# Kernel tuning notes

Measured on AMD Instinct MI355X. Metric: run time of the kernel, lower is better.

Reference implementation:

```python
import jax, jax.numpy as jnp
import numpy as np

NUM_HEADS = 16
THRESHOLD = 0.1  # default forward arg; with seq_len > 2**max_qubits the Grover path degenerates to probs > threshold


def setup_inputs() -> dict:
    key = jax.random.key(0)
    ks = jax.random.split(key, 5)
    B, S, E = 4, 1024, 1024
    return {
        "x": jax.random.normal(ks[0], (B, S, E), dtype=jnp.float32),
        "w_qkv": jax.random.normal(ks[1], (E, 3 * E), dtype=jnp.float32) * (E ** -0.5),
        "b_qkv": jax.random.normal(ks[2], (3 * E,), dtype=jnp.float32) * 0.02,
        "w_proj": jax.random.normal(ks[3], (E, E), dtype=jnp.float32) * (E ** -0.5),
        "b_proj": jax.random.normal(ks[4], (E,), dtype=jnp.float32) * 0.02,
    }


def reference(x, w_qkv, b_qkv, w_proj, b_proj):
    B, S, E = x.shape
    H = NUM_HEADS
    Dh = E // H
    scale = Dh ** -0.5
    # qkv projection -> [3, B, H, S, Dh]
    qkv = (x @ w_qkv + b_qkv).reshape(B, S, 3, H, Dh).transpose(2, 0, 3, 1, 4)
    q, k, v = qkv[0], qkv[1], qkv[2]
    attn_logits = jnp.einsum("bhqd,bhkd->bhqk", q, k) * scale  # [B,H,S,S]
    attn_probs = jax.nn.softmax(attn_logits, axis=-1)
    # Grover filter degenerates to threshold mask for S > 2**max_qubits
    mask = attn_probs > THRESHOLD
    any_selected = jnp.any(mask, axis=-1, keepdims=True)
    # fallback: keep only the argmax column in rows where nothing passed threshold
    fallback = jax.nn.one_hot(jnp.argmax(attn_probs, axis=-1), S, dtype=jnp.bool_)
    mask = jnp.where(any_selected, mask, fallback)
    filtered_logits = jnp.where(mask, attn_logits, -jnp.inf)
    filtered_attn = jax.nn.softmax(filtered_logits, axis=-1)
    # dropout is identity in eval / p=0
    out = jnp.einsum("bhqk,bhkd->bhqd", filtered_attn, v)  # [B,H,S,Dh]
    out = out.transpose(0, 2, 1, 3).reshape(B, S, E)
    out = out @ w_proj + b_proj
    return out, filtered_attn
```

## Files before the change

kernel.cpp:

```cpp
#include <hip/hip_runtime.h>
#include <math.h>

#define SS 1024
#define OUT0_SZ (4*1024*1024)

typedef _Float16 f16;
typedef _Float16 h8 __attribute__((ext_vector_type(8)));
typedef _Float16 h4 __attribute__((ext_vector_type(4)));
typedef float f32x4 __attribute__((ext_vector_type(4)));

#define MFMA(a,b,c) __builtin_amdgcn_mfma_f32_16x16x32_f16(a, b, c, 0, 0, 0)

__device__ __forceinline__ void gload_lds16(const void* g, void* l) {
  __builtin_amdgcn_global_load_lds((const __attribute__((address_space(1))) void*)g,
                                   (__attribute__((address_space(3))) void*)l, 16, 0, 0);
}

template<int SPLIT>
__global__ __launch_bounds__(256)
void transpose_split(const float* __restrict__ in, f16* __restrict__ outHi,
                     f16* __restrict__ outLo, int K, int N, float scale) {
  __shared__ float t[32][33];
  const int n0 = blockIdx.x * 32, k0 = blockIdx.y * 32;
  const int tx = threadIdx.x & 31, ty = threadIdx.x >> 5;
#pragma unroll
  for (int j = 0; j < 4; j++)
    t[ty + j * 8][tx] = in[(size_t)(k0 + ty + j * 8) * N + n0 + tx] * scale;
  __syncthreads();
#pragma unroll
  for (int j = 0; j < 4; j++) {
    float v = t[tx][ty + j * 8];
    f16 h = (f16)v;
    size_t idx = (size_t)(n0 + ty + j * 8) * K + k0 + tx;
    outHi[idx] = h;
    if (SPLIT) outLo[idx] = (f16)(v - (float)h);
  }
}

__global__ __launch_bounds__(256)
void transpose_v(const f16* __restrict__ in, f16* __restrict__ out) {
  __shared__ f16 t[32][33];
  const int bh = blockIdx.z, s0 = blockIdx.x * 32, d0 = blockIdx.y * 32;
  in  += (size_t)bh * 65536;
  out += (size_t)bh * 65536;
  const int tx = threadIdx.x & 31, ty = threadIdx.x >> 5;
#pragma unroll
  for (int j = 0; j < 4; j++)
    t[ty + j * 8][tx] = in[(size_t)(s0 + ty + j * 8) * 64 + d0 + tx];
  __syncthreads();
#pragma unroll
  for (int j = 0; j < 4; j++)
    out[(size_t)(d0 + ty + j * 8) * 1024 + s0 + tx] = t[tx][ty + j * 8];
}

__global__ __launch_bounds__(256)
void qkv_gemm(const float* __restrict__ x, const f16* __restrict__ WhiT,
              const f16* __restrict__ WloT, const float* __restrict__ bias,
              f16* __restrict__ Qhi, f16* __restrict__ Qlo,
              f16* __restrict__ Khi, f16* __restrict__ Klo, f16* __restrict__ Vf) {
  __shared__ __align__(16) f16 Ah[128 * 32], Al[128 * 32], Bh[128 * 32], Bl[128 * 32];
  const int tid = threadIdx.x, w = tid >> 6, l = tid & 63;
  const int n0 = blockIdx.x * 128, m0 = blockIdx.y * 128;
  const int wr = (w & 1) * 64, wc = (w >> 1) * 64;
  const int fr = l & 15, fq = l >> 4;
  f32x4 acc[4][4] = {};

  for (int kt = 0; kt < 1024; kt += 32) {
    __syncthreads();
#pragma unroll
    for (int i = 0; i < 2; i++) {
      int row = w * 32 + i * 16 + (l >> 2);
      size_t srcoff = (size_t)(n0 + row) * 1024 + kt + (l & 3) * 8;
      gload_lds16(WhiT + srcoff, Bh + w * 1024 + i * 512);
      gload_lds16(WloT + srcoff, Bl + w * 1024 + i * 512);
    }
#pragma unroll
    for (int r4 = 0; r4 < 4; r4++) {
      int f = r4 * 256 + tid;
      int row = f >> 3, c4 = (f & 7) * 4;
      float4 xv = *(const float4*)&x[(size_t)(m0 + row) * 1024 + kt + c4];
      float vv[4] = {xv.x, xv.y, xv.z, xv.w};
      h4 hh, ll;
#pragma unroll
      for (int j = 0; j < 4; j++) {
        float sv = vv[j] * 64.f;
        f16 h = (f16)sv;
        hh[j] = h; ll[j] = (f16)(sv - (float)h);
      }
      *(h4*)&Ah[row * 32 + c4] = hh;
      *(h4*)&Al[row * 32 + c4] = ll;
    }
    __syncthreads();
    h8 ah[4], al[4], bh[4], bl[4];
#pragma unroll
    for (int m = 0; m < 4; m++) {
      ah[m] = *(h8*)&Ah[(wr + m * 16 + fr) * 32 + fq * 8];
      al[m] = *(h8*)&Al[(wr + m * 16 + fr) * 32 + fq * 8];
    }
#pragma unroll
    for (int n = 0; n < 4; n++) {
      bh[n] = *(h8*)&Bh[(wc + n * 16 + fr) * 32 + fq * 8];
      bl[n] = *(h8*)&Bl[(wc + n * 16 + fr) * 32 + fq * 8];
    }
#pragma unroll
    for (int m = 0; m < 4; m++)
#pragma unroll
      for (int n = 0; n < 4; n++) {
        acc[m][n] = MFMA(ah[m], bh[n], acc[m][n]);
        acc[m][n] = MFMA(al[m], bh[n], acc[m][n]);
        acc[m][n] = MFMA(ah[m], bl[n], acc[m][n]);
      }
  }

#pragma unroll
  for (int m = 0; m < 4; m++)
#pragma unroll
    for (int n = 0; n < 4; n++)
#pragma unroll
      for (int j = 0; j < 4; j++) {
        int row = m0 + wr + m * 16 + fq * 4 + j;
        int col = n0 + wc + n * 16 + fr;
        float val = acc[m][n][j] * (1.f / 262144.f) + bias[col];
        int t = col >> 10, h = (col >> 6) & 15, d = col & 63;
        int b = row >> 10, s = row & 1023;
        size_t idx = ((size_t)(b * 16 + h) * 1024 + s) * 64 + d;
        if (t == 0) { f16 hh = (f16)(val * 64.f); Qhi[idx] = hh; Qlo[idx] = (f16)(val * 64.f - (float)hh); }
        else if (t == 1) { f16 hh = (f16)(val * 64.f); Khi[idx] = hh; Klo[idx] = (f16)(val * 64.f - (float)hh); }
        else Vf[idx] = (f16)val;
      }
}

__global__ __launch_bounds__(256)
void qk_gemm(const f16* __restrict__ Qhi, const f16* __restrict__ Qlo,
             const f16* __restrict__ Khi, const f16* __restrict__ Klo,
             float* __restrict__ att) {
  __shared__ __align__(16) f16 Ah[128 * 32], Al[128 * 32], Bh[128 * 32], Bl[128 * 32];
  const int bh = blockIdx.z;
  const size_t off = (size_t)bh * 65536;
  const int tid = threadIdx.x, w = tid >> 6, l = tid & 63;
  const int n0 = blockIdx.x * 128, m0 = blockIdx.y * 128;
  const int wr = (w & 1) * 64, wc = (w >> 1) * 64;
  const int fr = l & 15, fq = l >> 4;
  f32x4 acc[4][4] = {};

  for (int kt = 0; kt < 64; kt += 32) {
    __syncthreads();
#pragma unroll
    for (int i = 0; i < 2; i++) {
      int row = w * 32 + i * 16 + (l >> 2);
      int co = kt + (l & 3) * 8;
      gload_lds16(Qhi + off + (size_t)(m0 + row) * 64 + co, Ah + w * 1024 + i * 512);
      gload_lds16(Qlo + off + (size_t)(m0 + row) * 64 + co, Al + w * 1024 + i * 512);
      gload_lds16(Khi + off + (size_t)(n0 + row) * 64 + co, Bh + w * 1024 + i * 512);
      gload_lds16(Klo + off + (size_t)(n0 + row) * 64 + co, Bl + w * 1024 + i * 512);
    }
    __syncthreads();
    h8 ah[4], al[4], bh[4], bl[4];
#pragma unroll
    for (int m = 0; m < 4; m++) {
      ah[m] = *(h8*)&Ah[(wr + m * 16 + fr) * 32 + fq * 8];
      al[m] = *(h8*)&Al[(wr + m * 16 + fr) * 32 + fq * 8];
    }
#pragma unroll
    for (int n = 0; n < 4; n++) {
      bh[n] = *(h8*)&Bh[(wc + n * 16 + fr) * 32 + fq * 8];
      bl[n] = *(h8*)&Bl[(wc + n * 16 + fr) * 32 + fq * 8];
    }
#pragma unroll
    for (int m = 0; m < 4; m++)
#pragma unroll
      for (int n = 0; n < 4; n++) {
        acc[m][n] = MFMA(ah[m], bh[n], acc[m][n]);
        acc[m][n] = MFMA(al[m], bh[n], acc[m][n]);
        acc[m][n] = MFMA(ah[m], bl[n], acc[m][n]);
      }
  }

  float* L = att + (size_t)bh * 1048576;
#pragma unroll
  for (int m = 0; m < 4; m++)
#pragma unroll
    for (int n = 0; n < 4; n++)
#pragma unroll
      for (int j = 0; j < 4; j++) {
        int row = m0 + wr + m * 16 + fq * 4 + j;
        int col = n0 + wc + n * 16 + fr;
        L[(size_t)row * 1024 + col] = acc[m][n][j] * (1.f / 32768.f);
      }
}

__global__ __launch_bounds__(256)
void softmax_filter(float* __restrict__ att) {
  float* p = att + (size_t)blockIdx.x * SS;
  const int tid = threadIdx.x;
  const int lane = tid & 63, wv = tid >> 6;

  float4 z4 = *(const float4*)&p[tid * 4];
  float z[4] = {z4.x, z4.y, z4.z, z4.w};

  float m = z[0]; int am = tid * 4;
#pragma unroll
  for (int j = 1; j < 4; j++) if (z[j] > m) { m = z[j]; am = tid * 4 + j; }
#pragma unroll
  for (int off = 32; off >= 1; off >>= 1) {
    float om = __shfl_xor(m, off, 64);
    int oa = __shfl_xor(am, off, 64);
    if (om > m || (om == m && oa < am)) { m = om; am = oa; }
  }
  __shared__ float wm[4]; __shared__ int wa[4];
  __shared__ float wsum[4]; __shared__ float wf[4]; __shared__ int wany[4];
  if (lane == 0) { wm[wv] = m; wa[wv] = am; }
  __syncthreads();
  m = wm[0]; am = wa[0];
#pragma unroll
  for (int w = 1; w < 4; w++) {
    float om = wm[w]; int oa = wa[w];
    if (om > m || (om == m && oa < am)) { m = om; am = oa; }
  }

  float e[4]; float s = 0.f;
#pragma unroll
  for (int j = 0; j < 4; j++) { e[j] = expf(z[j] - m); s += e[j]; }
#pragma unroll
  for (int off = 32; off >= 1; off >>= 1) s += __shfl_xor(s, off, 64);
  if (lane == 0) wsum[wv] = s;
  __syncthreads();
  s = wsum[0] + wsum[1] + wsum[2] + wsum[3];

  bool sel[4]; float fl = 0.f; int anyl = 0;
#pragma unroll
  for (int j = 0; j < 4; j++) {
    sel[j] = (e[j] / s > 0.1f);
    if (sel[j]) { fl += e[j]; anyl = 1; }
  }
#pragma unroll
  for (int off = 32; off >= 1; off >>= 1) fl += __shfl_xor(fl, off, 64);
  int wany_l = __any(anyl);
  if (lane == 0) { wf[wv] = fl; wany[wv] = wany_l; }
  __syncthreads();
  float fs = wf[0] + wf[1] + wf[2] + wf[3];
  int any = wany[0] | wany[1] | wany[2] | wany[3];

  float4 fa;
  float* faf = (float*)&fa;
#pragma unroll
  for (int j = 0; j < 4; j++) {
    if (any) faf[j] = sel[j] ? e[j] / fs : 0.f;
    else     faf[j] = (tid * 4 + j == am) ? 1.f : 0.f;
  }
  *(float4*)&p[tid * 4] = fa;
}

__global__ __launch_bounds__(256)
void pv_gemm(const float* __restrict__ att, const f16* __restrict__ Vt,
             f16* __restrict__ ao) {
  __shared__ __align__(16) f16 A[128 * 32], B[64 * 32];
  const int bh = blockIdx.y, m0 = blockIdx.x * 128;
  const float* fa = att + (size_t)bh * 1048576;
  const f16* Vb = Vt + (size_t)bh * 65536;
  const int tid = threadIdx.x, w = tid >> 6, l = tid & 63;
  const int wr = (w & 1) * 64, wc = (w >> 1) * 32;
  const int fr = l & 15, fq = l >> 4;
  f32x4 acc[4][2] = {};

  for (int kt = 0; kt < 1024; kt += 32) {
    __syncthreads();
    {
      int row = w * 16 + (l >> 2);
      gload_lds16(Vb + (size_t)row * 1024 + kt + (l & 3) * 8, B + w * 512);
    }
#pragma unroll
    for (int r4 = 0; r4 < 4; r4++) {
      int f = r4 * 256 + tid;
      int row = f >> 3, c4 = (f & 7) * 4;
      float4 pv4 = *(const float4*)&fa[(size_t)(m0 + row) * 1024 + kt + c4];
      h4 hh;
      hh[0] = (f16)pv4.x; hh[1] = (f16)pv4.y; hh[2] = (f16)pv4.z; hh[3] = (f16)pv4.w;
      *(h4*)&A[row * 32 + c4] = hh;
    }
    __syncthreads();
    h8 a[4], b[2];
#pragma unroll
    for (int m = 0; m < 4; m++) a[m] = *(h8*)&A[(wr + m * 16 + fr) * 32 + fq * 8];
#pragma unroll
    for (int n = 0; n < 2; n++) b[n] = *(h8*)&B[(wc + n * 16 + fr) * 32 + fq * 8];
#pragma unroll
    for (int m = 0; m < 4; m++)
#pragma unroll
      for (int n = 0; n < 2; n++) acc[m][n] = MFMA(a[m], b[n], acc[m][n]);
  }

  const int b = bh >> 4, h = bh & 15;
#pragma unroll
  for (int m = 0; m < 4; m++)
#pragma unroll
    for (int n = 0; n < 2; n++)
#pragma unroll
      for (int j = 0; j < 4; j++) {
        int s = m0 + wr + m * 16 + fq * 4 + j;
        int d = wc + n * 16 + fr;
        ao[((size_t)(b * 1024 + s)) * 1024 + h * 64 + d] = (f16)acc[m][n][j];
      }
}

__global__ __launch_bounds__(256)
void proj_gemm(const f16* __restrict__ ao, const f16* __restrict__ WpT,
               const float* __restrict__ bias, float* __restrict__ out) {
  __shared__ __align__(16) f16 A[128 * 32], B[128 * 32];
  const int tid = threadIdx.x, w = tid >> 6, l = tid & 63;
  const int n0 = blockIdx.x * 128, m0 = blockIdx.y * 128;
  const int wr = (w & 1) * 64, wc = (w >> 1) * 64;
  const int fr = l & 15, fq = l >> 4;
  f32x4 acc[4][4] = {};

  for (int kt = 0; kt < 1024; kt += 32) {
    __syncthreads();
#pragma unroll
    for (int i = 0; i < 2; i++) {
      int row = w * 32 + i * 16 + (l >> 2);
      gload_lds16(ao  + (size_t)(m0 + row) * 1024 + kt + (l & 3) * 8, A + w * 1024 + i * 512);
      gload_lds16(WpT + (size_t)(n0 + row) * 1024 + kt + (l & 3) * 8, B + w * 1024 + i * 512);
    }
    __syncthreads();
    h8 a[4], b[4];
#pragma unroll
    for (int m = 0; m < 4; m++) a[m] = *(h8*)&A[(wr + m * 16 + fr) * 32 + fq * 8];
#pragma unroll
    for (int n = 0; n < 4; n++) b[n] = *(h8*)&B[(wc + n * 16 + fr) * 32 + fq * 8];
#pragma unroll
    for (int m = 0; m < 4; m++)
#pragma unroll
      for (int n = 0; n < 4; n++) acc[m][n] = MFMA(a[m], b[n], acc[m][n]);
  }

#pragma unroll
  for (int m = 0; m < 4; m++)
#pragma unroll
    for (int n = 0; n < 4; n++)
#pragma unroll
      for (int j = 0; j < 4; j++) {
        int row = m0 + wr + m * 16 + fq * 4 + j;
        int col = n0 + wc + n * 16 + fr;
        out[(size_t)row * 1024 + col] = acc[m][n][j] + bias[col];
      }
}

extern "C" void kernel_launch(void* const* d_in, const int* in_sizes, int n_in,
                              void* d_out, int out_size, void* d_ws, size_t ws_size,
                              hipStream_t stream) {
  const float* x      = (const float*)d_in[0];
  const float* w_qkv  = (const float*)d_in[1];
  const float* b_qkv  = (const float*)d_in[2];
  const float* w_proj = (const float*)d_in[3];
  const float* b_proj = (const float*)d_in[4];

  float* out0 = (float*)d_out;
  float* att  = out0 + OUT0_SZ;

  f16* ws16 = (f16*)d_ws;
  f16* WhiT = ws16;
  f16* WloT = ws16 +  3145728;
  f16* WpT  = ws16 +  6291456;
  f16* Qhi  = ws16 +  7340032;
  f16* Qlo  = ws16 + 11534336;
  f16* Khi  = ws16 + 15728640;
  f16* Klo  = ws16 + 19922944;
  f16* Vf   = ws16 + 24117248;
  f16* Vt   = ws16 + 28311552;
  f16* ao16 = ws16;

  transpose_split<1><<<dim3(96, 32), 256, 0, stream>>>(w_qkv, WhiT, WloT, 1024, 3072, 4096.f);
  transpose_split<0><<<dim3(32, 32), 256, 0, stream>>>(w_proj, WpT, nullptr, 1024, 1024, 1.f);
  qkv_gemm<<<dim3(24, 32), 256, 0, stream>>>(x, WhiT, WloT, b_qkv, Qhi, Qlo, Khi, Klo, Vf);
  transpose_v<<<dim3(32, 2, 64), 256, 0, stream>>>(Vf, Vt);
  qk_gemm<<<dim3(8, 8, 64), 256, 0, stream>>>(Qhi, Qlo, Khi, Klo, att);
  softmax_filter<<<64 * SS, 256, 0, stream>>>(att);
  pv_gemm<<<dim3(8, 64), 256, 0, stream>>>(att, Vt, ao16);
  proj_gemm<<<dim3(8, 32), 256, 0, stream>>>(ao16, WpT, b_proj, out0);
}
```

Before: 661.4 us.

## Fuse QK^T with softmax filter in LDS and pre-split x to fp16

Replaces the separate QK^T GEMM and row softmax/threshold kernels with one kernel. It computes a 32-row stripe of logits into LDS, using swizzled K tiles, and then does the softmax, threshold and argmax fallback in place before writing the attention matrix once. This removes a full fp32 write and re-read of the 256 MB logits tensor. Separately, x is split into hi/lo fp16 buffers by a new pre-kernel, staged in the attention output region, so qkv_gemm can use direct global-to-LDS loads instead of converting inside the loop. The fused kernel uses a large LDS footprint (about 148 KB), which limits occupancy.

```diff
diff --git a/kernel.cpp b/kernel.cpp
--- a/kernel.cpp
+++ b/kernel.cpp
@@ -38,6 +38,22 @@
 }
 
 __global__ __launch_bounds__(256)
+void splitx(const float* __restrict__ x, f16* __restrict__ hi, f16* __restrict__ lo) {
+  const size_t i4 = (size_t)blockIdx.x * 256 + threadIdx.x;
+  float4 v = ((const float4*)x)[i4];
+  float vv[4] = {v.x, v.y, v.z, v.w};
+  h4 hh, ll;
+#pragma unroll
+  for (int j = 0; j < 4; j++) {
+    float sv = vv[j] * 64.f;
+    f16 h = (f16)sv;
+    hh[j] = h; ll[j] = (f16)(sv - (float)h);
+  }
+  ((h4*)hi)[i4] = hh;
+  ((h4*)lo)[i4] = ll;
+}
+
+__global__ __launch_bounds__(256)
 void transpose_v(const f16* __restrict__ in, f16* __restrict__ out) {
   __shared__ f16 t[32][33];
   const int bh = blockIdx.z, s0 = blockIdx.x * 32, d0 = blockIdx.y * 32;
@@ -54,8 +70,9 @@
 }
 
 __global__ __launch_bounds__(256)
-void qkv_gemm(const float* __restrict__ x, const f16* __restrict__ WhiT,
-              const f16* __restrict__ WloT, const float* __restrict__ bias,
+void qkv_gemm(const f16* __restrict__ Xhi, const f16* __restrict__ Xlo,
+              const f16* __restrict__ WhiT, const f16* __restrict__ WloT,
+              const float* __restrict__ bias,
               f16* __restrict__ Qhi, f16* __restrict__ Qlo,
               f16* __restrict__ Khi, f16* __restrict__ Klo, f16* __restrict__ Vf) {
   __shared__ __align__(16) f16 Ah[128 * 32], Al[128 * 32], Bh[128 * 32], Bl[128 * 32];
@@ -70,25 +87,13 @@
 #pragma unroll
     for (int i = 0; i < 2; i++) {
       int row = w * 32 + i * 16 + (l >> 2);
-      size_t srcoff = (size_t)(n0 + row) * 1024 + kt + (l & 3) * 8;
-      gload_lds16(WhiT + srcoff, Bh + w * 1024 + i * 512);
-      gload_lds16(WloT + srcoff, Bl + w * 1024 + i * 512);
-    }
-#pragma unroll
-    for (int r4 = 0; r4 < 4; r4++) {
-      int f = r4 * 256 + tid;
-      int row = f >> 3, c4 = (f & 7) * 4;
-      float4 xv = *(const float4*)&x[(size_t)(m0 + row) * 1024 + kt + c4];
-      float vv[4] = {xv.x, xv.y, xv.z, xv.w};
-      h4 hh, ll;
-#pragma unroll
-      for (int j = 0; j < 4; j++) {
-        float sv = vv[j] * 64.f;
-        f16 h = (f16)sv;
-        hh[j] = h; ll[j] = (f16)(sv - (float)h);
-      }
-      *(h4*)&Ah[row * 32 + c4] = hh;
-      *(h4*)&Al[row * 32 + c4] = ll;
+      int co = kt + (l & 3) * 8;
+      size_t aoff = (size_t)(m0 + row) * 1024 + co;
+      size_t boff = (size_t)(n0 + row) * 1024 + co;
+      gload_lds16(Xhi  + aoff, Ah + w * 1024 + i * 512);
+      gload_lds16(Xlo  + aoff, Al + w * 1024 + i * 512);
+      gload_lds16(WhiT + boff, Bh + w * 1024 + i * 512);
+      gload_lds16(WloT + boff, Bl + w * 1024 + i * 512);
     }
     __syncthreads();
     h8 ah[4], al[4], bh[4], bl[4];
@@ -131,124 +136,102 @@
 }
 
 __global__ __launch_bounds__(256)
-void qk_gemm(const f16* __restrict__ Qhi, const f16* __restrict__ Qlo,
-             const f16* __restrict__ Khi, const f16* __restrict__ Klo,
-             float* __restrict__ att) {
-  __shared__ __align__(16) f16 Ah[128 * 32], Al[128 * 32], Bh[128 * 32], Bl[128 * 32];
-  const int bh = blockIdx.z;
+void qksm(const f16* __restrict__ Qhi, const f16* __restrict__ Qlo,
+          const f16* __restrict__ Khi, const f16* __restrict__ Klo,
+          float* __restrict__ att) {
+  __shared__ float P[32][1028];
+  __shared__ __align__(16) f16 KH[4096], KL[4096];
+  const int bh = blockIdx.y, m0 = blockIdx.x * 32;
   const size_t off = (size_t)bh * 65536;
   const int tid = threadIdx.x, w = tid >> 6, l = tid & 63;
-  const int n0 = blockIdx.x * 128, m0 = blockIdx.y * 128;
-  const int wr = (w & 1) * 64, wc = (w >> 1) * 64;
   const int fr = l & 15, fq = l >> 4;
-  f32x4 acc[4][4] = {};
-
-  for (int kt = 0; kt < 64; kt += 32) {
-    __syncthreads();
-#pragma unroll
-    for (int i = 0; i < 2; i++) {
-      int row = w * 32 + i * 16 + (l >> 2);
-      int co = kt + (l & 3) * 8;
-      gload_lds16(Qhi + off + (size_t)(m0 + row) * 64 + co, Ah + w * 1024 + i * 512);
-      gload_lds16(Qlo + off + (size_t)(m0 + row) * 64 + co, Al + w * 1024 + i * 512);
-      gload_lds16(Khi + off + (size_t)(n0 + row) * 64 + co, Bh + w * 1024 + i * 512);
-      gload_lds16(Klo + off + (size_t)(n0 + row) * 64 + co, Bl + w * 1024 + i * 512);
-    }
-    __syncthreads();
-    h8 ah[4], al[4], bh[4], bl[4];
-#pragma unroll
-    for (int m = 0; m < 4; m++) {
-      ah[m] = *(h8*)&Ah[(wr + m * 16 + fr) * 32 + fq * 8];
-      al[m] = *(h8*)&Al[(wr + m * 16 + fr) * 32 + fq * 8];
-    }
-#pragma unroll
-    for (int n = 0; n < 4; n++) {
-      bh[n] = *(h8*)&Bh[(wc + n * 16 + fr) * 32 + fq * 8];
-      bl[n] = *(h8*)&Bl[(wc + n * 16 + fr) * 32 + fq * 8];
-    }
-#pragma unroll
-    for (int m = 0; m < 4; m++)
-#pragma unroll
-      for (int n = 0; n < 4; n++) {
-        acc[m][n] = MFMA(ah[m], bh[n], acc[m][n]);
-        acc[m][n] = MFMA(al[m], bh[n], acc[m][n]);
-        acc[m][n] = MFMA(ah[m], bl[n], acc[m][n]);
-      }
-  }
-
-  float* L = att + (size_t)bh * 1048576;
-#pragma unroll
-  for (int m = 0; m < 4; m++)
-#pragma unroll
-    for (int n = 0; n < 4; n++)
-#pragma unroll
-      for (int j = 0; j < 4; j++) {
-        int row = m0 + wr + m * 16 + fq * 4 + j;
-        int col = n0 + wc + n * 16 + fr;
-        L[(size_t)row * 1024 + col] = acc[m][n][j] * (1.f / 32768.f);
-      }
-}
-
-__global__ __launch_bounds__(256)
-void softmax_filter(float* __restrict__ att) {
-  float* p = att + (size_t)blockIdx.x * SS;
-  const int tid = threadIdx.x;
-  const int lane = tid & 63, wv = tid >> 6;
-
-  float4 z4 = *(const float4*)&p[tid * 4];
-  float z[4] = {z4.x, z4.y, z4.z, z4.w};
-
-  float m = z[0]; int am = tid * 4;
-#pragma unroll
-  for (int j = 1; j < 4; j++) if (z[j] > m) { m = z[j]; am = tid * 4 + j; }
-#pragma unroll
-  for (int off = 32; off >= 1; off >>= 1) {
-    float om = __shfl_xor(m, off, 64);
-    int oa = __shfl_xor(am, off, 64);
-    if (om > m || (om == m && oa < am)) { m = om; am = oa; }
-  }
-  __shared__ float wm[4]; __shared__ int wa[4];
-  __shared__ float wsum[4]; __shared__ float wf[4]; __shared__ int wany[4];
-  if (lane == 0) { wm[wv] = m; wa[wv] = am; }
-  __syncthreads();
-  m = wm[0]; am = wa[0];
-#pragma unroll
-  for (int w = 1; w < 4; w++) {
-    float om = wm[w]; int oa = wa[w];
-    if (om > m || (om == m && oa < am)) { m = om; am = oa; }
-  }
-
-  float e[4]; float s = 0.f;
-#pragma unroll
-  for (int j = 0; j < 4; j++) { e[j] = expf(z[j] - m); s += e[j]; }
-#pragma unroll
-  for (int off = 32; off >= 1; off >>= 1) s += __shfl_xor(s, off, 64);
-  if (lane == 0) wsum[wv] = s;
-  __syncthreads();
-  s = wsum[0] + wsum[1] + wsum[2] + wsum[3];
-
-  bool sel[4]; float fl = 0.f; int anyl = 0;
-#pragma unroll
-  for (int j = 0; j < 4; j++) {
-    sel[j] = (e[j] / s > 0.1f);
-    if (sel[j]) { fl += e[j]; anyl = 1; }
-  }
-#pragma unroll
-  for (int off = 32; off >= 1; off >>= 1) fl += __shfl_xor(fl, off, 64);
-  int wany_l = __any(anyl);
-  if (lane == 0) { wf[wv] = fl; wany[wv] = wany_l; }
-  __syncthreads();
-  float fs = wf[0] + wf[1] + wf[2] + wf[3];
-  int any = wany[0] | wany[1] | wany[2] | wany[3];
-
-  float4 fa;
-  float* faf = (float*)&fa;
-#pragma unroll
-  for (int j = 0; j < 4; j++) {
-    if (any) faf[j] = sel[j] ? e[j] / fs : 0.f;
-    else     faf[j] = (tid * 4 + j == am) ? 1.f : 0.f;
-  }
-  *(float4*)&p[tid * 4] = fa;
+  const int nw = w * 16;
+
+  h8 qh[2][2], ql[2][2];
+#pragma unroll
+  for (int m = 0; m < 2; m++)
+#pragma unroll
+    for (int kk = 0; kk < 2; kk++) {
+      size_t o = off + (size_t)(m0 + 16 * m + fr) * 64 + kk * 32 + fq * 8;
+      qh[m][kk] = *(const h8*)(Qhi + o);
+      ql[m][kk] = *(const h8*)(Qlo + o);
+    }
+
+  const char* KhiB = (const char*)(Khi + off);
+  const char* KloB = (const char*)(Klo + off);
+
+  for (int c = 0; c < 16; c++) {
+    {
+      int i0 = w * 2;
+#pragma unroll
+      for (int i = i0; i < i0 + 2; i++) {
+        int r = i * 8 + (l >> 3);
+        size_t gb = (size_t)(c * 64 + r) * 128 + (size_t)(((l & 7) * 16) ^ ((r & 7) << 4));
+        gload_lds16(KhiB + gb, (char*)KH + i * 1024);
+        gload_lds16(KloB + gb, (char*)KL + i * 1024);
+      }
+    }
+    __syncthreads();
+    f32x4 acc[2] = {};
+    const int R = nw + fr;
+    const int rs = (R & 7) << 4;
+#pragma unroll
+    for (int kk = 0; kk < 2; kk++) {
+      h8 b_h = *(const h8*)((const char*)KH + R * 128 + ((kk * 64 + fq * 16) ^ rs));
+      h8 b_l = *(const h8*)((const char*)KL + R * 128 + ((kk * 64 + fq * 16) ^ rs));
+#pragma unroll
+      for (int m = 0; m < 2; m++) {
+        acc[m] = MFMA(qh[m][kk], b_h, acc[m]);
+        acc[m] = MFMA(ql[m][kk], b_h, acc[m]);
+        acc[m] = MFMA(qh[m][kk], b_l, acc[m]);
+      }
+    }
+#pragma unroll
+    for (int m = 0; m < 2; m++)
+#pragma unroll
+      for (int j = 0; j < 4; j++)
+        P[16 * m + fq * 4 + j][c * 64 + nw + fr] = acc[m][j] * (1.f / 32768.f);
+    __syncthreads();
+  }
+
+  const int r0 = w * 8;
+  for (int rr = 0; rr < 8; rr++) {
+    const int r = r0 + rr;
+    float z[16];
+#pragma unroll
+    for (int i = 0; i < 16; i++) z[i] = P[r][l + 64 * i];
+    float m = z[0]; int am = l;
+#pragma unroll
+    for (int i = 1; i < 16; i++) { int idx = l + 64 * i; if (z[i] > m) { m = z[i]; am = idx; } }
+#pragma unroll
+    for (int o = 32; o >= 1; o >>= 1) {
+      float om = __shfl_xor(m, o, 64);
+      int oa = __shfl_xor(am, o, 64);
+      if (om > m || (om == m && oa < am)) { m = om; am = oa; }
+    }
+    float e[16]; float s = 0.f;
+#pragma unroll
+    for (int i = 0; i < 16; i++) { e[i] = expf(z[i] - m); s += e[i]; }
+#pragma unroll
+    for (int o = 32; o >= 1; o >>= 1) s += __shfl_xor(s, o, 64);
+    bool sel[16]; float fl = 0.f; int anyl = 0;
+#pragma unroll
+    for (int i = 0; i < 16; i++) {
+      sel[i] = (e[i] / s > 0.1f);
+      if (sel[i]) { fl += e[i]; anyl = 1; }
+    }
+#pragma unroll
+    for (int o = 32; o >= 1; o >>= 1) fl += __shfl_xor(fl, o, 64);
+    int any = __any(anyl);
+    float* arow = att + ((size_t)bh << 20) + (size_t)(m0 + r) * 1024;
+#pragma unroll
+    for (int i = 0; i < 16; i++) {
+      float v;
+      if (any) v = sel[i] ? e[i] / fl : 0.f;
+      else     v = ((l + 64 * i) == am) ? 1.f : 0.f;
+      arow[l + 64 * i] = v;
+    }
+  }
 }
 
 __global__ __launch_bounds__(256)
@@ -356,6 +339,9 @@
 
   float* out0 = (float*)d_out;
   float* att  = out0 + OUT0_SZ;
+
+  f16* Xhi = (f16*)att;
+  f16* Xlo = Xhi + 4194304;
 
   f16* ws16 = (f16*)d_ws;
   f16* WhiT = ws16;
@@ -371,10 +357,10 @@
 
   transpose_split<1><<<dim3(96, 32), 256, 0, stream>>>(w_qkv, WhiT, WloT, 1024, 3072, 4096.f);
   transpose_split<0><<<dim3(32, 32), 256, 0, stream>>>(w_proj, WpT, nullptr, 1024, 1024, 1.f);
-  qkv_gemm<<<dim3(24, 32), 256, 0, stream>>>(x, WhiT, WloT, b_qkv, Qhi, Qlo, Khi, Klo, Vf);
+  splitx<<<4096, 256, 0, stream>>>(x, Xhi, Xlo);
+  qkv_gemm<<<dim3(24, 32), 256, 0, stream>>>(Xhi, Xlo, WhiT, WloT, b_qkv, Qhi, Qlo, Khi, Klo, Vf);
   transpose_v<<<dim3(32, 2, 64), 256, 0, stream>>>(Vf, Vt);
-  qk_gemm<<<dim3(8, 8, 64), 256, 0, stream>>>(Qhi, Qlo, Khi, Klo, att);
-  softmax_filter<<<64 * SS, 256, 0, stream>>>(att);
+  qksm<<<dim3(32, 64), 256, 0, stream>>>(Qhi, Qlo, Khi, Klo, att);
   pv_gemm<<<dim3(8, 64), 256, 0, stream>>>(att, Vt, ao16);
   proj_gemm<<<dim3(8, 32), 256, 0, stream>>>(ao16, WpT, b_proj, out0);
 }
```

Measured after the change: 727.0 us. +9.9%, slower.
